# Kernel tuning notes

Hardware: AMD Instinct MI355X
Metric: run time of the kernel (lower is better)

The kernel has to match this reference:

```python
import jax, jax.numpy as jnp
import numpy as np

NUM_TOKENS = 2048
NUM_EXPERTS = 8
TOPK = 2
INTERMEDIATE = 2048
HIDDEN = 1024


def setup_inputs() -> dict:
    key = jax.random.key(0)
    k1, k2, k3 = jax.random.split(key, 3)
    intermediate_states = jax.random.normal(k1, (NUM_TOKENS * TOPK, INTERMEDIATE), dtype=jnp.float32)
    # per-expert down-projection, scaled like a typical init
    w = jax.random.normal(k2, (NUM_EXPERTS, INTERMEDIATE, HIDDEN), dtype=jnp.float32) / np.float32(np.sqrt(INTERMEDIATE))
    router_logits = jax.random.normal(k3, (NUM_TOKENS, NUM_EXPERTS), dtype=jnp.float32)
    return {"intermediate_states": intermediate_states, "w": w, "router_logits": router_logits}


def reference(intermediate_states, w, router_logits):
    T, E = router_logits.shape
    K = TOPK
    H = w.shape[-1]
    # Routing: softmax over experts, then top-k weights/ids (precompute_ctx.full_topk_weight/full_topk_ids)
    probs = jax.nn.softmax(router_logits, axis=-1)          # [T, E]
    topk_w, topk_ids = jax.lax.top_k(probs, K)              # [T, K]
    # Grouped expert GEMM: each (token, k) row is multiplied by its expert's weight.
    # Compute against all experts once, then gather the routed expert per row.
    out_all = jnp.einsum('ri,eih->reh', intermediate_states, w)   # [T*K, E, H]
    flat_ids = topk_ids.reshape(-1)                               # [T*K]
    routed = jnp.take_along_axis(out_all, flat_ids[:, None, None], axis=1)[:, 0, :]  # [T*K, H]
    # topk-weighted reduction over the K expert outputs per token
    out = (routed.reshape(T, K, H) * topk_w[..., None]).sum(axis=1)  # [T, H]
    # reduce-scatter across tensor-parallel ranks: with world_size=1 this is identity
    return out
```

## Files before the change

kernel.cpp:

```cpp
#include <hip/hip_runtime.h>

#define T_TOKENS 2048
#define N_EXPERTS 8
#define ROWS (T_TOKENS * 2)
#define I_DIM 2048
#define H_DIM 1024

#define M_TILE 64
#define N_TILE 128
#define BK 64
#define KSPLIT 2
#define KCHUNK (I_DIM / KSPLIT)

typedef __bf16 bf16x8 __attribute__((ext_vector_type(8)));
typedef float f32x4 __attribute__((ext_vector_type(4)));

__device__ inline void load_lds16(const void* g, void* l) {
    __builtin_amdgcn_global_load_lds(
        (const __attribute__((address_space(1))) void*)g,
        (__attribute__((address_space(3))) void*)l, 16, 0, 0);
}

__global__ __launch_bounds__(256) void prep_kernel(
    const float* __restrict__ w, const float* __restrict__ x,
    __bf16* __restrict__ wT, __bf16* __restrict__ xB,
    float* __restrict__ out, int* __restrict__ cnt) {
    const int b = blockIdx.x;
    const int t = threadIdx.x;
    if (b < 2048) {
        __shared__ float tile[128 * 65];
        const int e = b >> 8;
        const int k0 = ((b >> 4) & 15) * 128;
        const int n0 = (b & 15) * 64;
        const float* ws = w + (size_t)e * (I_DIM * H_DIM) + (size_t)k0 * H_DIM + n0;
#pragma unroll
        for (int i = 0; i < 8; ++i) {
            int flat = i * 256 + t;
            int k = flat >> 4, nq = (flat & 15) * 4;
            f32x4 v = *(const f32x4*)(ws + (size_t)k * H_DIM + nq);
            float* d = &tile[k * 65 + nq];
            d[0] = v.x; d[1] = v.y; d[2] = v.z; d[3] = v.w;
        }
        __syncthreads();
        __bf16* wd = wT + (size_t)e * (H_DIM * I_DIM) + (size_t)n0 * I_DIM + k0;
#pragma unroll
        for (int j = 0; j < 4; ++j) {
            int flat = j * 256 + t;
            int n = flat >> 4, kc = (flat & 15) * 8;
            bf16x8 o;
#pragma unroll
            for (int q = 0; q < 8; ++q) o[q] = (__bf16)tile[(kc + q) * 65 + n];
            *(bf16x8*)(wd + (size_t)n * I_DIM + kc) = o;
        }
    } else if (b < 4096) {
        size_t base = ((size_t)(b - 2048) * 256 + t) * 16;
        const f32x4* xs = (const f32x4*)(x + base);
        f32x4 v0 = xs[0], v1 = xs[1], v2 = xs[2], v3 = xs[3];
        bf16x8 o0 = { (__bf16)v0.x, (__bf16)v0.y, (__bf16)v0.z, (__bf16)v0.w,
                      (__bf16)v1.x, (__bf16)v1.y, (__bf16)v1.z, (__bf16)v1.w };
        bf16x8 o1 = { (__bf16)v2.x, (__bf16)v2.y, (__bf16)v2.z, (__bf16)v2.w,
                      (__bf16)v3.x, (__bf16)v3.y, (__bf16)v3.z, (__bf16)v3.w };
        *(bf16x8*)(xB + base) = o0;
        *(bf16x8*)(xB + base + 8) = o1;
    } else {
        size_t idx = (size_t)(b - 4096) * 256 + t;
        f32x4 z = (f32x4){0.f, 0.f, 0.f, 0.f};
        ((f32x4*)out)[2 * idx] = z;
        ((f32x4*)out)[2 * idx + 1] = z;
        if (b == 4096 && t < N_EXPERTS) cnt[t] = 0;
    }
}

__global__ void routing_kernel(const float* __restrict__ logits,
                               float* __restrict__ topk_w,
                               int* __restrict__ cnt,
                               int* __restrict__ rowlist) {
    int t = blockIdx.x * blockDim.x + threadIdx.x;
    if (t >= T_TOKENS) return;
    float l[8];
#pragma unroll
    for (int e = 0; e < 8; ++e) l[e] = logits[t * 8 + e];
    float mx = l[0];
#pragma unroll
    for (int e = 1; e < 8; ++e) mx = fmaxf(mx, l[e]);
    float s = 0.f;
#pragma unroll
    for (int e = 0; e < 8; ++e) { l[e] = expf(l[e] - mx); s += l[e]; }
    float inv = 1.f / s;
    float v0 = -1.f, v1 = -1.f; int i0 = 0, i1 = 0;
#pragma unroll
    for (int e = 0; e < 8; ++e) {
        float p = l[e] * inv;
        if (p > v0)      { v1 = v0; i1 = i0; v0 = p; i0 = e; }
        else if (p > v1) { v1 = p; i1 = e; }
    }
    topk_w[2 * t]     = v0;
    topk_w[2 * t + 1] = v1;
    int p0 = atomicAdd(&cnt[i0], 1); rowlist[i0 * ROWS + p0] = 2 * t;
    int p1 = atomicAdd(&cnt[i1], 1); rowlist[i1 * ROWS + p1] = 2 * t + 1;
}

__global__ __launch_bounds__(256, 4) void gemm_kernel(
    const __bf16* __restrict__ xB, const __bf16* __restrict__ wT,
    const int* __restrict__ cnt, const int* __restrict__ rowlist,
    const float* __restrict__ topk_w, float* __restrict__ out) {
    const int e = blockIdx.y;
    const int cnt_e = cnt[e];
    const int m0 = blockIdx.z * M_TILE;
    if (m0 >= cnt_e) return;
    const int ntile = blockIdx.x & 7;
    const int khalf = blockIdx.x >> 3;
    const int n0 = ntile * N_TILE;
    const int tid = threadIdx.x;
    const int lane = tid & 63;
    const int wave = tid >> 6;
    const int wm = wave & 1, wn = wave >> 1;

    __shared__ __bf16 As[M_TILE * BK];
    __shared__ __bf16 Bs[N_TILE * BK];

    const int* rl = rowlist + e * ROWS;

    const int lc = lane & 7;
    const int lr = lane >> 3;
    const int cg = lc ^ lr;

    const int ar0 = 16 * wave + lr;
    int gm0 = m0 + ar0;     if (gm0 >= cnt_e) gm0 = cnt_e - 1;
    int gm1 = m0 + ar0 + 8; if (gm1 >= cnt_e) gm1 = cnt_e - 1;
    const __bf16* asrc0 = xB + (size_t)rl[gm0] * I_DIM + khalf * KCHUNK + cg * 8;
    const __bf16* asrc1 = xB + (size_t)rl[gm1] * I_DIM + khalf * KCHUNK + cg * 8;
    __bf16* adst0 = As + 1024 * wave;
    __bf16* adst1 = As + 1024 * wave + 512;

    const int br = 32 * wave + lr;
    const __bf16* wTe = wT + (size_t)e * (H_DIM * I_DIM);
    const __bf16* bsrc = wTe + (size_t)(n0 + br) * I_DIM + khalf * KCHUNK + cg * 8;
    __bf16* bdst = Bs + 2048 * wave;

    const int lm = lane & 15, lg = lane >> 4, sw = lm & 7;
    int offA[2][2], offB[2][4];
#pragma unroll
    for (int s = 0; s < 2; ++s) {
        int cs = (((s * 4) + lg) ^ sw) * 8;
#pragma unroll
        for (int mt = 0; mt < 2; ++mt)
            offA[s][mt] = (wm * 32 + mt * 16 + lm) * BK + cs;
#pragma unroll
        for (int nt = 0; nt < 4; ++nt)
            offB[s][nt] = (wn * 64 + nt * 16 + lm) * BK + cs;
    }

    f32x4 acc[2][4];
#pragma unroll
    for (int mt = 0; mt < 2; ++mt)
#pragma unroll
        for (int nt = 0; nt < 4; ++nt)
            acc[mt][nt] = (f32x4){0.f, 0.f, 0.f, 0.f};

    for (int ks = 0; ks < KCHUNK; ks += BK) {
        __syncthreads();
        load_lds16(asrc0, adst0);
        load_lds16(asrc1, adst1);
        load_lds16(bsrc,              bdst);
        load_lds16(bsrc +  8 * I_DIM, bdst + 512);
        load_lds16(bsrc + 16 * I_DIM, bdst + 1024);
        load_lds16(bsrc + 24 * I_DIM, bdst + 1536);
        asrc0 += BK; asrc1 += BK; bsrc += BK;
        __syncthreads();

#pragma unroll
        for (int s = 0; s < 2; ++s) {
            bf16x8 a0 = *(const bf16x8*)&As[offA[s][0]];
            bf16x8 a1 = *(const bf16x8*)&As[offA[s][1]];
            bf16x8 b0 = *(const bf16x8*)&Bs[offB[s][0]];
            bf16x8 b1 = *(const bf16x8*)&Bs[offB[s][1]];
            bf16x8 b2 = *(const bf16x8*)&Bs[offB[s][2]];
            bf16x8 b3 = *(const bf16x8*)&Bs[offB[s][3]];
            acc[0][0] = __builtin_amdgcn_mfma_f32_16x16x32_bf16(a0, b0, acc[0][0], 0, 0, 0);
            acc[0][1] = __builtin_amdgcn_mfma_f32_16x16x32_bf16(a0, b1, acc[0][1], 0, 0, 0);
            acc[0][2] = __builtin_amdgcn_mfma_f32_16x16x32_bf16(a0, b2, acc[0][2], 0, 0, 0);
            acc[0][3] = __builtin_amdgcn_mfma_f32_16x16x32_bf16(a0, b3, acc[0][3], 0, 0, 0);
            acc[1][0] = __builtin_amdgcn_mfma_f32_16x16x32_bf16(a1, b0, acc[1][0], 0, 0, 0);
            acc[1][1] = __builtin_amdgcn_mfma_f32_16x16x32_bf16(a1, b1, acc[1][1], 0, 0, 0);
            acc[1][2] = __builtin_amdgcn_mfma_f32_16x16x32_bf16(a1, b2, acc[1][2], 0, 0, 0);
            acc[1][3] = __builtin_amdgcn_mfma_f32_16x16x32_bf16(a1, b3, acc[1][3], 0, 0, 0);
        }
    }

    const int lq = lane >> 4, ln = lane & 15;
#pragma unroll
    for (int mt = 0; mt < 2; ++mt) {
#pragma unroll
        for (int j = 0; j < 4; ++j) {
            int gm = m0 + wm * 32 + mt * 16 + lq * 4 + j;
            if (gm < cnt_e) {
                int row = rl[gm];
                float tw = topk_w[row];
                float* orow = out + (size_t)(row >> 1) * H_DIM + n0 + wn * 64 + ln;
#pragma unroll
                for (int nt = 0; nt < 4; ++nt)
                    atomicAdd(&orow[nt * 16], acc[mt][nt][j] * tw);
            }
        }
    }
}

extern "C" void kernel_launch(void* const* d_in, const int* in_sizes, int n_in,
                              void* d_out, int out_size, void* d_ws, size_t ws_size,
                              hipStream_t stream) {
    const float* x      = (const float*)d_in[0];
    const float* w      = (const float*)d_in[1];
    const float* logits = (const float*)d_in[2];
    float* out = (float*)d_out;

    char* ws = (char*)d_ws;
    float*  topk_w  = (float*)ws;
    int*    cnt     = (int*)(ws + 16384);
    int*    rowlist = (int*)(ws + 16384 + 128);
    __bf16* wT      = (__bf16*)(ws + 16384 + 128 + 131072);
    __bf16* xB      = (__bf16*)(ws + 16384 + 128 + 131072 + 33554432);

    prep_kernel<<<5120, 256, 0, stream>>>(w, x, wT, xB, out, cnt);
    routing_kernel<<<T_TOKENS / 256, 256, 0, stream>>>(logits, topk_w, cnt, rowlist);
    gemm_kernel<<<dim3((H_DIM / N_TILE) * KSPLIT, N_EXPERTS, ROWS / M_TILE), 256, 0, stream>>>(
        xB, wT, cnt, rowlist, topk_w, out);
}
```

Before: 196.1 us.

## Double-buffer GEMM LDS tiles, enlarge M tile, fuse routing into prep kernel

The GEMM now uses 128-row M tiles, so each wave computes a 4x4 grid of MFMA fragments instead of 2x4. It double-buffers the A/B LDS tiles so the next k-step's global-to-LDS loads run while the current step's MFMAs execute, with one barrier per step. Routing moves into an extra block of the prep kernel that keeps counts in LDS, removing a kernel launch and the global atomics. The costs are fewer GEMM blocks, lower occupancy (launch bounds 2), more LDS and registers, and serial routing of all tokens in a single block.

```diff
diff --git a/kernel.cpp b/kernel.cpp
--- a/kernel.cpp
+++ b/kernel.cpp
@@ -6,11 +6,12 @@
 #define I_DIM 2048
 #define H_DIM 1024
 
-#define M_TILE 64
+#define M_TILE 128
 #define N_TILE 128
 #define BK 64
 #define KSPLIT 2
 #define KCHUNK (I_DIM / KSPLIT)
+#define NSTEP (KCHUNK / BK)
 
 typedef __bf16 bf16x8 __attribute__((ext_vector_type(8)));
 typedef float f32x4 __attribute__((ext_vector_type(4)));
@@ -23,8 +24,10 @@
 
 __global__ __launch_bounds__(256) void prep_kernel(
     const float* __restrict__ w, const float* __restrict__ x,
+    const float* __restrict__ logits,
     __bf16* __restrict__ wT, __bf16* __restrict__ xB,
-    float* __restrict__ out, int* __restrict__ cnt) {
+    float* __restrict__ out, float* __restrict__ topk_w,
+    int* __restrict__ cnt, int* __restrict__ rowlist) {
     const int b = blockIdx.x;
     const int t = threadIdx.x;
     if (b < 2048) {
@@ -62,45 +65,46 @@
                       (__bf16)v3.x, (__bf16)v3.y, (__bf16)v3.z, (__bf16)v3.w };
         *(bf16x8*)(xB + base) = o0;
         *(bf16x8*)(xB + base + 8) = o1;
-    } else {
+    } else if (b < 5120) {
         size_t idx = (size_t)(b - 4096) * 256 + t;
         f32x4 z = (f32x4){0.f, 0.f, 0.f, 0.f};
         ((f32x4*)out)[2 * idx] = z;
         ((f32x4*)out)[2 * idx + 1] = z;
-        if (b == 4096 && t < N_EXPERTS) cnt[t] = 0;
-    }
-}
-
-__global__ void routing_kernel(const float* __restrict__ logits,
-                               float* __restrict__ topk_w,
-                               int* __restrict__ cnt,
-                               int* __restrict__ rowlist) {
-    int t = blockIdx.x * blockDim.x + threadIdx.x;
-    if (t >= T_TOKENS) return;
-    float l[8];
-#pragma unroll
-    for (int e = 0; e < 8; ++e) l[e] = logits[t * 8 + e];
-    float mx = l[0];
-#pragma unroll
-    for (int e = 1; e < 8; ++e) mx = fmaxf(mx, l[e]);
-    float s = 0.f;
-#pragma unroll
-    for (int e = 0; e < 8; ++e) { l[e] = expf(l[e] - mx); s += l[e]; }
-    float inv = 1.f / s;
-    float v0 = -1.f, v1 = -1.f; int i0 = 0, i1 = 0;
-#pragma unroll
-    for (int e = 0; e < 8; ++e) {
-        float p = l[e] * inv;
-        if (p > v0)      { v1 = v0; i1 = i0; v0 = p; i0 = e; }
-        else if (p > v1) { v1 = p; i1 = e; }
-    }
-    topk_w[2 * t]     = v0;
-    topk_w[2 * t + 1] = v1;
-    int p0 = atomicAdd(&cnt[i0], 1); rowlist[i0 * ROWS + p0] = 2 * t;
-    int p1 = atomicAdd(&cnt[i1], 1); rowlist[i1 * ROWS + p1] = 2 * t + 1;
-}
-
-__global__ __launch_bounds__(256, 4) void gemm_kernel(
+    } else {
+        __shared__ int lcnt[N_EXPERTS];
+        if (t < N_EXPERTS) lcnt[t] = 0;
+        __syncthreads();
+#pragma unroll
+        for (int i = 0; i < 8; ++i) {
+            int tok = i * 256 + t;
+            float l[8];
+#pragma unroll
+            for (int e = 0; e < 8; ++e) l[e] = logits[tok * 8 + e];
+            float mx = l[0];
+#pragma unroll
+            for (int e = 1; e < 8; ++e) mx = fmaxf(mx, l[e]);
+            float s = 0.f;
+#pragma unroll
+            for (int e = 0; e < 8; ++e) { l[e] = expf(l[e] - mx); s += l[e]; }
+            float inv = 1.f / s;
+            float v0 = -1.f, v1 = -1.f; int i0 = 0, i1 = 0;
+#pragma unroll
+            for (int e = 0; e < 8; ++e) {
+                float p = l[e] * inv;
+                if (p > v0)      { v1 = v0; i1 = i0; v0 = p; i0 = e; }
+                else if (p > v1) { v1 = p; i1 = e; }
+            }
+            topk_w[2 * tok]     = v0;
+            topk_w[2 * tok + 1] = v1;
+            int p0 = atomicAdd(&lcnt[i0], 1); rowlist[i0 * ROWS + p0] = 2 * tok;
+            int p1 = atomicAdd(&lcnt[i1], 1); rowlist[i1 * ROWS + p1] = 2 * tok + 1;
+        }
+        __syncthreads();
+        if (t < N_EXPERTS) cnt[t] = lcnt[t];
+    }
+}
+
+__global__ __launch_bounds__(256, 2) void gemm_kernel(
     const __bf16* __restrict__ xB, const __bf16* __restrict__ wT,
     const int* __restrict__ cnt, const int* __restrict__ rowlist,
     const float* __restrict__ topk_w, float* __restrict__ out) {
@@ -116,8 +120,8 @@
     const int wave = tid >> 6;
     const int wm = wave & 1, wn = wave >> 1;
 
-    __shared__ __bf16 As[M_TILE * BK];
-    __shared__ __bf16 Bs[N_TILE * BK];
+    __shared__ __bf16 As[2][M_TILE * BK];
+    __shared__ __bf16 Bs[2][N_TILE * BK];
 
     const int* rl = rowlist + e * ROWS;
 
@@ -125,75 +129,79 @@
     const int lr = lane >> 3;
     const int cg = lc ^ lr;
 
-    const int ar0 = 16 * wave + lr;
-    int gm0 = m0 + ar0;     if (gm0 >= cnt_e) gm0 = cnt_e - 1;
-    int gm1 = m0 + ar0 + 8; if (gm1 >= cnt_e) gm1 = cnt_e - 1;
-    const __bf16* asrc0 = xB + (size_t)rl[gm0] * I_DIM + khalf * KCHUNK + cg * 8;
-    const __bf16* asrc1 = xB + (size_t)rl[gm1] * I_DIM + khalf * KCHUNK + cg * 8;
-    __bf16* adst0 = As + 1024 * wave;
-    __bf16* adst1 = As + 1024 * wave + 512;
-
-    const int br = 32 * wave + lr;
+    const __bf16* asrc[4];
+#pragma unroll
+    for (int i = 0; i < 4; ++i) {
+        int gm = m0 + 32 * wave + 8 * i + lr;
+        if (gm >= cnt_e) gm = cnt_e - 1;
+        asrc[i] = xB + (size_t)rl[gm] * I_DIM + khalf * KCHUNK + cg * 8;
+    }
     const __bf16* wTe = wT + (size_t)e * (H_DIM * I_DIM);
-    const __bf16* bsrc = wTe + (size_t)(n0 + br) * I_DIM + khalf * KCHUNK + cg * 8;
-    __bf16* bdst = Bs + 2048 * wave;
+    const __bf16* bsrc = wTe + (size_t)(n0 + 32 * wave + lr) * I_DIM
+                             + khalf * KCHUNK + cg * 8;
 
     const int lm = lane & 15, lg = lane >> 4, sw = lm & 7;
-    int offA[2][2], offB[2][4];
+    int offA[2][4], offB[2][4];
 #pragma unroll
     for (int s = 0; s < 2; ++s) {
         int cs = (((s * 4) + lg) ^ sw) * 8;
 #pragma unroll
-        for (int mt = 0; mt < 2; ++mt)
-            offA[s][mt] = (wm * 32 + mt * 16 + lm) * BK + cs;
-#pragma unroll
-        for (int nt = 0; nt < 4; ++nt)
-            offB[s][nt] = (wn * 64 + nt * 16 + lm) * BK + cs;
-    }
-
-    f32x4 acc[2][4];
-#pragma unroll
-    for (int mt = 0; mt < 2; ++mt)
+        for (int f = 0; f < 4; ++f) {
+            offA[s][f] = (wm * 64 + f * 16 + lm) * BK + cs;
+            offB[s][f] = (wn * 64 + f * 16 + lm) * BK + cs;
+        }
+    }
+
+    f32x4 acc[4][4];
+#pragma unroll
+    for (int mt = 0; mt < 4; ++mt)
 #pragma unroll
         for (int nt = 0; nt < 4; ++nt)
             acc[mt][nt] = (f32x4){0.f, 0.f, 0.f, 0.f};
 
-    for (int ks = 0; ks < KCHUNK; ks += BK) {
-        __syncthreads();
-        load_lds16(asrc0, adst0);
-        load_lds16(asrc1, adst1);
-        load_lds16(bsrc,              bdst);
-        load_lds16(bsrc +  8 * I_DIM, bdst + 512);
-        load_lds16(bsrc + 16 * I_DIM, bdst + 1024);
-        load_lds16(bsrc + 24 * I_DIM, bdst + 1536);
-        asrc0 += BK; asrc1 += BK; bsrc += BK;
-        __syncthreads();
-
+#pragma unroll
+    for (int i = 0; i < 4; ++i) {
+        load_lds16(asrc[i], &As[0][(32 * wave + 8 * i) * BK]);
+        load_lds16(bsrc + (size_t)(8 * i) * I_DIM, &Bs[0][(32 * wave + 8 * i) * BK]);
+    }
+    __syncthreads();
+
+    for (int tstep = 0; tstep < NSTEP; ++tstep) {
+        const int cur = tstep & 1;
+        if (tstep + 1 < NSTEP) {
+            const int koff = (tstep + 1) * BK;
+#pragma unroll
+            for (int i = 0; i < 4; ++i) {
+                load_lds16(asrc[i] + koff, &As[cur ^ 1][(32 * wave + 8 * i) * BK]);
+                load_lds16(bsrc + (size_t)(8 * i) * I_DIM + koff,
+                           &Bs[cur ^ 1][(32 * wave + 8 * i) * BK]);
+            }
+        }
+        const __bf16* Ab = As[cur];
+        const __bf16* Bb = Bs[cur];
 #pragma unroll
         for (int s = 0; s < 2; ++s) {
-            bf16x8 a0 = *(const bf16x8*)&As[offA[s][0]];
-            bf16x8 a1 = *(const bf16x8*)&As[offA[s][1]];
-            bf16x8 b0 = *(const bf16x8*)&Bs[offB[s][0]];
-            bf16x8 b1 = *(const bf16x8*)&Bs[offB[s][1]];
-            bf16x8 b2 = *(const bf16x8*)&Bs[offB[s][2]];
-            bf16x8 b3 = *(const bf16x8*)&Bs[offB[s][3]];
-            acc[0][0] = __builtin_amdgcn_mfma_f32_16x16x32_bf16(a0, b0, acc[0][0], 0, 0, 0);
-            acc[0][1] = __builtin_amdgcn_mfma_f32_16x16x32_bf16(a0, b1, acc[0][1], 0, 0, 0);
-            acc[0][2] = __builtin_amdgcn_mfma_f32_16x16x32_bf16(a0, b2, acc[0][2], 0, 0, 0);
-            acc[0][3] = __builtin_amdgcn_mfma_f32_16x16x32_bf16(a0, b3, acc[0][3], 0, 0, 0);
-            acc[1][0] = __builtin_amdgcn_mfma_f32_16x16x32_bf16(a1, b0, acc[1][0], 0, 0, 0);
-            acc[1][1] = __builtin_amdgcn_mfma_f32_16x16x32_bf16(a1, b1, acc[1][1], 0, 0, 0);
-            acc[1][2] = __builtin_amdgcn_mfma_f32_16x16x32_bf16(a1, b2, acc[1][2], 0, 0, 0);
-            acc[1][3] = __builtin_amdgcn_mfma_f32_16x16x32_bf16(a1, b3, acc[1][3], 0, 0, 0);
-        }
+            bf16x8 af[4], bfr[4];
+#pragma unroll
+            for (int f = 0; f < 4; ++f) af[f] = *(const bf16x8*)&Ab[offA[s][f]];
+#pragma unroll
+            for (int f = 0; f < 4; ++f) bfr[f] = *(const bf16x8*)&Bb[offB[s][f]];
+#pragma unroll
+            for (int mt = 0; mt < 4; ++mt)
+#pragma unroll
+                for (int nt = 0; nt < 4; ++nt)
+                    acc[mt][nt] = __builtin_amdgcn_mfma_f32_16x16x32_bf16(
+                        af[mt], bfr[nt], acc[mt][nt], 0, 0, 0);
+        }
+        __syncthreads();
     }
 
     const int lq = lane >> 4, ln = lane & 15;
 #pragma unroll
-    for (int mt = 0; mt < 2; ++mt) {
+    for (int mt = 0; mt < 4; ++mt) {
 #pragma unroll
         for (int j = 0; j < 4; ++j) {
-            int gm = m0 + wm * 32 + mt * 16 + lq * 4 + j;
+            int gm = m0 + wm * 64 + mt * 16 + lq * 4 + j;
             if (gm < cnt_e) {
                 int row = rl[gm];
                 float tw = topk_w[row];
@@ -221,8 +229,7 @@
     __bf16* wT      = (__bf16*)(ws + 16384 + 128 + 131072);
     __bf16* xB      = (__bf16*)(ws + 16384 + 128 + 131072 + 33554432);
 
-    prep_kernel<<<5120, 256, 0, stream>>>(w, x, wT, xB, out, cnt);
-    routing_kernel<<<T_TOKENS / 256, 256, 0, stream>>>(logits, topk_w, cnt, rowlist);
+    prep_kernel<<<5121, 256, 0, stream>>>(w, x, logits, wT, xB, out, topk_w, cnt, rowlist);
     gemm_kernel<<<dim3((H_DIM / N_TILE) * KSPLIT, N_EXPERTS, ROWS / M_TILE), 256, 0, stream>>>(
         xB, wT, cnt, rowlist, topk_w, out);
 }
```

Measured after the change: 199.2 us. No clear change (+1.6%).
